# Performance work log

Measured on AMD Instinct MI355X. Metric: run time of the kernel, lower is better.

## Reference

```python
import jax, jax.numpy as jnp
import numpy as np

B, S, H, NH = 32, 512, 768, 12
EC, EU = 4, 4
CAP = 1.0
DH = H // NH
CAPACITY = int(CAP * B / EC)  # Switch-style capacity per common expert


def setup_inputs() -> dict:
    key = jax.random.key(0)
    ks = jax.random.split(key, 10)
    s = 0.02
    E = EC + EU  # experts stacked: [0:EC]=common, [EC:]=unique
    return {
        "hidden_states": jax.random.normal(ks[0], (B, S, H), jnp.float32),
        "attention_mask": jnp.zeros((B, S), jnp.float32),  # additive mask
        "Wq": jax.random.normal(ks[1], (E, H, H), jnp.float32) * s,
        "bq": jnp.zeros((E, H), jnp.float32),
        "Wk": jax.random.normal(ks[2], (E, H, H), jnp.float32) * s,
        "bk": jnp.zeros((E, H), jnp.float32),
        "Wv": jax.random.normal(ks[3], (E, H, H), jnp.float32) * s,
        "bv": jnp.zeros((E, H), jnp.float32),
        "Wo": jax.random.normal(ks[4], (E, H, H), jnp.float32) * s,
        "bo": jnp.zeros((E, H), jnp.float32),
        "Wsc": jax.random.normal(ks[5], (H, EC), jnp.float32) * s,
        "bsc": jnp.zeros((EC,), jnp.float32),
        "Wsu": jax.random.normal(ks[6], (H, EU), jnp.float32) * s,
        "bsu": jnp.zeros((EU,), jnp.float32),
    }


def reference(hidden_states, attention_mask, Wq, bq, Wk, bk, Wv, bv, Wo, bo,
              Wsc, bsc, Wsu, bsu):
    # ---- common routing (per-sequence top-1 over mean-pooled tokens) ----
    h_mean = hidden_states.mean(axis=1)                       # [B,H]
    pc = jax.nn.softmax(h_mean @ Wsc + bsc, axis=-1)          # [B,EC]
    rc = jnp.argmax(pc, axis=-1)                              # [B]
    pc_max = jnp.max(pc, axis=-1)                             # [B]
    # capacity drop: within each expert keep the CAPACITY highest-prob seqs
    order = jnp.argsort(-pc_max)                              # global desc sort
    oh = jax.nn.one_hot(rc[order], EC, dtype=jnp.int32)       # [B,EC]
    rank = jnp.take_along_axis(jnp.cumsum(oh, axis=0), rc[order][:, None], 1)[:, 0]
    kept = jnp.zeros((B,), bool).at[order].set(rank <= CAPACITY)

    # ---- unique routing for dropped sequences (mean is per-sequence, so
    #      computing on the full batch and masking matches torch) ----
    pu = jax.nn.softmax(h_mean @ Wsu + bsu, axis=-1)          # [B,EU]
    ru = jnp.argmax(pu, axis=-1)
    pu_max = jnp.max(pu, axis=-1)

    # per-sequence expert index into stacked [EC+EU] expert params
    eidx = jnp.where(kept, rc, EC + ru)                       # [B]
    # scaling factor p/stop_grad(p): ==1 in fwd, routes grads to the gate
    scale = jnp.where(kept,
                      pc_max / jax.lax.stop_gradient(pc_max),
                      pu_max / jax.lax.stop_gradient(pu_max))

    # ---- gather-dispatch: per-sequence expert weights ----
    Wq_b, Wk_b, Wv_b, Wo_b = Wq[eidx], Wk[eidx], Wv[eidx], Wo[eidx]  # [B,H,H]
    bq_b, bk_b, bv_b, bo_b = bq[eidx], bk[eidx], bv[eidx], bo[eidx]  # [B,H]

    def heads(t):  # [B,S,H] -> [B,NH,S,DH]
        return t.reshape(B, S, NH, DH).transpose(0, 2, 1, 3)

    q = heads(jnp.einsum('bsh,bhd->bsd', hidden_states, Wq_b) + bq_b[:, None, :])
    k = heads(jnp.einsum('bsh,bhd->bsd', hidden_states, Wk_b) + bk_b[:, None, :])
    v = heads(jnp.einsum('bsh,bhd->bsd', hidden_states, Wv_b) + bv_b[:, None, :])

    scores = jnp.einsum('bhsd,bhtd->bhst', q, k) / np.float32(np.sqrt(DH))
    scores = scores + attention_mask[:, None, None, :]        # additive mask
    attn = jax.nn.softmax(scores, axis=-1)
    ctx = jnp.einsum('bhst,bhtd->bhsd', attn, v)
    ctx = ctx.transpose(0, 2, 1, 3).reshape(B, S, H)

    out = jnp.einsum('bsh,bhd->bsd', ctx, Wo_b) + bo_b[:, None, :]
    return out * scale[:, None, None]
```

## Files before the change

kernel.cpp:

```cpp
#include <hip/hip_runtime.h>
#include <hip/hip_bf16.h>

#define B_ 32
#define S_ 512
#define H_ 768
#define NH_ 12
#define DH_ 64
#define EC_ 4
#define CAPN_ 8

using short8  = __attribute__((ext_vector_type(8))) short;
using floatx4 = __attribute__((ext_vector_type(4))) float;
using uint2v  = __attribute__((ext_vector_type(2))) unsigned;
using bf16 = __hip_bfloat16;

__device__ __forceinline__ void gl_lds16(const void* g, void* l) {
  __builtin_amdgcn_global_load_lds(
      (const __attribute__((address_space(1))) unsigned int*)g,
      (__attribute__((address_space(3))) unsigned int*)l, 16, 0, 0);
}

__device__ __forceinline__ unsigned pk2(float lo, float hi) {
  __hip_bfloat162 h = __float22bfloat162_rn(make_float2(lo, hi));
  unsigned r;
  __builtin_memcpy(&r, &h, 4);
  return r;
}

__global__ void k_mean_convert(const float* __restrict__ X, bf16* __restrict__ Xh,
                               float* __restrict__ partial) {
  int idx = blockIdx.x * 256 + threadIdx.x;
  int b = idx / H_, h = idx - b * H_;
  int s0 = blockIdx.y * 64;
  size_t base = ((size_t)b * S_ + s0) * H_ + h;
  float sum = 0.f;
#pragma unroll 8
  for (int s = 0; s < 64; ++s) {
    float v = X[base + (size_t)s * H_];
    Xh[base + (size_t)s * H_] = __float2bfloat16(v);
    sum += v;
  }
  partial[(size_t)blockIdx.y * (B_ * H_) + idx] = sum;
}

__global__ void k_mean_reduce(const float* __restrict__ partial, float* __restrict__ hmean) {
  int idx = blockIdx.x * 256 + threadIdx.x;
  float s = 0.f;
#pragma unroll
  for (int c = 0; c < 8; ++c) s += partial[(size_t)c * (B_ * H_) + idx];
  hmean[idx] = s * (1.f / 512.f);
}

__global__ void k_wt(const float* __restrict__ Wq, const float* __restrict__ Wk,
                     const float* __restrict__ Wv, const float* __restrict__ Wo,
                     bf16* __restrict__ Wt) {
  __shared__ float tile[32][33];
  int z = blockIdx.z;
  const float* Wbase = (z < 8 ? Wq : z < 16 ? Wk : z < 24 ? Wv : Wo) + (size_t)(z & 7) * H_ * H_;
  int k0 = blockIdx.x * 32, n0 = blockIdx.y * 32;
  int tj = threadIdx.x & 31, ti = threadIdx.x >> 5;
#pragma unroll
  for (int r = 0; r < 4; ++r)
    tile[ti + r * 8][tj] = Wbase[(size_t)(k0 + ti + r * 8) * H_ + n0 + tj];
  __syncthreads();
  bf16* out = Wt + (size_t)z * H_ * H_;
#pragma unroll
  for (int r = 0; r < 4; ++r)
    out[(size_t)(n0 + ti + r * 8) * H_ + k0 + tj] = __float2bfloat16(tile[tj][ti + r * 8]);
}

__global__ void k_gate(const float* __restrict__ hmean,
                       const float* __restrict__ Wsc, const float* __restrict__ bsc,
                       const float* __restrict__ Wsu, const float* __restrict__ bsu,
                       float* __restrict__ logits) {
  int b = blockIdx.x;
  int t = threadIdx.x;
  int g = t >> 3, p = t & 7;
  const float* hm = hmean + (size_t)b * H_;
  const float* w;
  float bias;
  if (g < 4) { w = Wsc + g; bias = bsc[g]; }
  else       { w = Wsu + (g - 4); bias = bsu[g - 4]; }
  float acc = 0.f;
  for (int j = p; j < H_; j += 8) acc += hm[j] * w[j * 4];
  acc += __shfl_xor(acc, 1);
  acc += __shfl_xor(acc, 2);
  acc += __shfl_xor(acc, 4);
  if (p == 0) logits[b * 8 + g] = acc + bias;
}

__global__ void k_route2(const float* __restrict__ logits, int* __restrict__ eidx) {
  __shared__ float pcmax[B_];
  __shared__ int rc_s[B_], ru_s[B_];
  int t = threadIdx.x;
  if (t < B_) {
    float lg[8];
#pragma unroll
    for (int e = 0; e < 8; ++e) lg[e] = logits[t * 8 + e];
    float m = lg[0]; int a = 0;
    for (int e = 1; e < 4; ++e) if (lg[e] > m) { m = lg[e]; a = e; }
    float s = 0.f;
    for (int e = 0; e < 4; ++e) s += expf(lg[e] - m);
    pcmax[t] = 1.f / s;
    rc_s[t] = a;
    float mu = lg[4]; int au = 0;
    for (int e = 1; e < 4; ++e) if (lg[4 + e] > mu) { mu = lg[4 + e]; au = e; }
    ru_s[t] = au;
  }
  __syncthreads();
  if (t == 0) {
    bool used[B_], kept[B_];
    int cnt[EC_] = {0, 0, 0, 0};
    for (int i = 0; i < B_; ++i) used[i] = false;
    for (int i = 0; i < B_; ++i) {
      int best = 0; float bv = -1e30f;
      for (int j = 0; j < B_; ++j)
        if (!used[j] && pcmax[j] > bv) { bv = pcmax[j]; best = j; }
      used[best] = true;
      kept[best] = (++cnt[rc_s[best]] <= CAPN_);
    }
    for (int i = 0; i < B_; ++i)
      eidx[i] = kept[i] ? rc_s[i] : EC_ + ru_s[i];
  }
}

template <int OMODE>
__global__ __launch_bounds__(256) void k_gemm(
    const bf16* __restrict__ A, const bf16* __restrict__ Wt,
    const float* __restrict__ bias0, const float* __restrict__ bias1,
    const float* __restrict__ bias2,
    void* out0, void* out1, void* out2,
    const int* __restrict__ eidx, int mat0) {
  __shared__ __align__(16) char lds[2][32768];
  int bz = blockIdx.z;
  int b = blockIdx.y;
  int e = eidx[b];
  int mtile = blockIdx.x & 3, ntile = blockIdx.x >> 2;
  int m0 = mtile * 128, n0 = ntile * 128;
  const bf16* Ab = A + (size_t)b * S_ * H_;
  const bf16* Wb = Wt + (size_t)((mat0 + bz) * 8 + e) * H_ * H_;
  const float* bias = ((bz == 0) ? bias0 : (bz == 1) ? bias1 : bias2) + (size_t)e * H_;
  void* outp = (bz == 0) ? out0 : (bz == 1) ? out1 : out2;

  int t = threadIdx.x, lane = t & 63, w = t >> 6;
  int wm = (w & 1) * 64, wn = (w >> 1) * 64;
  int lm = lane & 15, lq = lane >> 4;

  auto stage = [&](int kt) {
    char* buf = lds[kt & 1];
#pragma unroll
    for (int r = 0; r < 8; ++r) {
      int c = t + r * 256;
      const bf16* g;
      if (c < 1024) {
        int mm = c >> 3, pos = c & 7, kc = pos ^ (mm & 7);
        g = Ab + (size_t)(m0 + mm) * H_ + kt * 64 + kc * 8;
      } else {
        int c2 = c - 1024;
        int nn = c2 >> 3, pos = c2 & 7, kc = pos ^ (nn & 7);
        g = Wb + (size_t)(n0 + nn) * H_ + kt * 64 + kc * 8;
      }
      gl_lds16(g, buf + (size_t)c * 16);
    }
  };

  floatx4 acc[4][4] = {};
  stage(0);
  __syncthreads();
  for (int kt = 0; kt < 12; ++kt) {
    if (kt < 11) stage(kt + 1);
    const char* cur = lds[kt & 1];
#pragma unroll
    for (int kf = 0; kf < 2; ++kf) {
      int kc = kf * 4 + lq;
      short8 af[4], bf[4];
#pragma unroll
      for (int mf = 0; mf < 4; ++mf) {
        int mm = wm + mf * 16 + lm;
        af[mf] = *(const short8*)(cur + ((size_t)(mm * 8 + (kc ^ (mm & 7)))) * 16);
      }
#pragma unroll
      for (int nf = 0; nf < 4; ++nf) {
        int nn = wn + nf * 16 + lm;
        bf[nf] = *(const short8*)(cur + 16384 + ((size_t)(nn * 8 + (kc ^ (nn & 7)))) * 16);
      }
#pragma unroll
      for (int mf = 0; mf < 4; ++mf)
#pragma unroll
        for (int nf = 0; nf < 4; ++nf)
          acc[mf][nf] = __builtin_amdgcn_mfma_f32_16x16x32_bf16(af[mf], bf[nf], acc[mf][nf], 0, 0, 0);
    }
    if (kt < 11) __syncthreads();
  }
#pragma unroll
  for (int mf = 0; mf < 4; ++mf) {
#pragma unroll
    for (int nf = 0; nf < 4; ++nf) {
      int n = n0 + wn + nf * 16 + lm;
      float bv = bias[n];
      int mrow = m0 + wm + mf * 16 + lq * 4;
      size_t rowbase = ((size_t)b * S_ + mrow) * H_ + n;
#pragma unroll
      for (int r = 0; r < 4; ++r) {
        float v = acc[mf][nf][r] + bv;
        if (OMODE == 0) {
          if (bz == 2) {
            int s = mrow + r;
            ((bf16*)outp)[((size_t)(b * NH_ + (n >> 6))) * 32768 +
                          (size_t)(s >> 3) * 512 + (n & 63) * 8 + (s & 7)] =
                __float2bfloat16(v);
          } else {
            ((bf16*)outp)[rowbase + (size_t)r * H_] = __float2bfloat16(v);
          }
        } else {
          ((float*)outp)[rowbase + (size_t)r * H_] = v;
        }
      }
    }
  }
}

__global__ __launch_bounds__(256, 3) void k_attn(
    const bf16* __restrict__ Q, const bf16* __restrict__ K,
    const bf16* __restrict__ Vt, const float* __restrict__ mask,
    bf16* __restrict__ Ctx) {
  int bh = blockIdx.x;
  int b = bh / NH_, h = bh - b * NH_;
  int t = threadIdx.x, lane = t & 63, w = t >> 6;
  int lm = lane & 15, lq = lane >> 4;
  int q0 = blockIdx.y * 128 + w * 32;

  short8 qf[2][2];
#pragma unroll
  for (int mf = 0; mf < 2; ++mf)
#pragma unroll
    for (int kf = 0; kf < 2; ++kf)
      qf[mf][kf] = *(const short8*)(Q + ((size_t)(b * S_ + q0 + mf * 16 + lm)) * H_ +
                                    h * DH_ + kf * 32 + lq * 8);

  int kr = ((lm >> 2) << 3) + (lm & 3);
  const int koff[4] = {0, 4, 32, 36};
  const bf16* kbase = K + ((size_t)(b * S_) + kr) * H_ + h * DH_ + lq * 8;
  const bf16* vtb = Vt + ((size_t)(b * NH_ + h)) * 32768;
  const float* mbase = mask + (size_t)b * S_ + lq * 8;

  floatx4 oacc[2][4] = {};
  float m_[2] = {-1e30f, -1e30f}, l_[2] = {0.f, 0.f};

  for (int kt = 0; kt < 8; ++kt) {
    floatx4 sT[2][4] = {};
#pragma unroll
    for (int kf = 0; kf < 2; ++kf) {
      short8 kb4[4];
#pragma unroll
      for (int nf = 0; nf < 4; ++nf)
        kb4[nf] = *(const short8*)(kbase + (size_t)(kt * 64 + koff[nf]) * H_ + kf * 32);
#pragma unroll
      for (int mf = 0; mf < 2; ++mf)
#pragma unroll
        for (int nf = 0; nf < 4; ++nf)
          sT[mf][nf] = __builtin_amdgcn_mfma_f32_16x16x32_bf16(kb4[nf], qf[mf][kf], sT[mf][nf], 0, 0, 0);
    }
    short8 vf[2][4];
#pragma unroll
    for (int kf = 0; kf < 2; ++kf)
#pragma unroll
      for (int nf = 0; nf < 4; ++nf)
        vf[kf][nf] = *(const short8*)(vtb + (size_t)(kt * 8 + kf * 4 + lq) * 512 +
                                      (nf * 16 + lm) * 8);
    const floatx4* mp = (const floatx4*)(mbase + kt * 64);
    floatx4 mv[4] = {mp[0], mp[1], mp[8], mp[9]};

    short8 pf[2][2];
#pragma unroll
    for (int mf = 0; mf < 2; ++mf) {
      float p[4][4];
#pragma unroll
      for (int nf = 0; nf < 4; ++nf)
#pragma unroll
        for (int r = 0; r < 4; ++r)
          p[nf][r] = sT[mf][nf][r] * 0.125f + mv[nf][r];
      float t01 = fmaxf(fmaxf(fmaxf(p[0][0], p[0][1]), fmaxf(p[0][2], p[0][3])),
                        fmaxf(fmaxf(p[1][0], p[1][1]), fmaxf(p[1][2], p[1][3])));
      float t23 = fmaxf(fmaxf(fmaxf(p[2][0], p[2][1]), fmaxf(p[2][2], p[2][3])),
                        fmaxf(fmaxf(p[3][0], p[3][1]), fmaxf(p[3][2], p[3][3])));
      float tm = fmaxf(t01, t23);
      tm = fmaxf(tm, __shfl_xor(tm, 16));
      tm = fmaxf(tm, __shfl_xor(tm, 32));
      float mn = fmaxf(m_[mf], tm);
      float a = __expf(m_[mf] - mn);
      m_[mf] = mn;
      float ps = 0.f;
#pragma unroll
      for (int nf = 0; nf < 4; ++nf)
#pragma unroll
        for (int r = 0; r < 4; ++r) {
          p[nf][r] = __expf(p[nf][r] - mn);
          ps += p[nf][r];
        }
      ps += __shfl_xor(ps, 16);
      ps += __shfl_xor(ps, 32);
      l_[mf] = l_[mf] * a + ps;
#pragma unroll
      for (int nf = 0; nf < 4; ++nf) oacc[mf][nf] *= a;
      union { short8 s8; unsigned u[4]; } pku;
      pku.u[0] = pk2(p[0][0], p[0][1]); pku.u[1] = pk2(p[0][2], p[0][3]);
      pku.u[2] = pk2(p[1][0], p[1][1]); pku.u[3] = pk2(p[1][2], p[1][3]);
      pf[mf][0] = pku.s8;
      pku.u[0] = pk2(p[2][0], p[2][1]); pku.u[1] = pk2(p[2][2], p[2][3]);
      pku.u[2] = pk2(p[3][0], p[3][1]); pku.u[3] = pk2(p[3][2], p[3][3]);
      pf[mf][1] = pku.s8;
    }
#pragma unroll
    for (int kf = 0; kf < 2; ++kf)
#pragma unroll
      for (int mf = 0; mf < 2; ++mf)
#pragma unroll
        for (int nf = 0; nf < 4; ++nf)
          oacc[mf][nf] = __builtin_amdgcn_mfma_f32_16x16x32_bf16(vf[kf][nf], pf[mf][kf], oacc[mf][nf], 0, 0, 0);
  }
#pragma unroll
  for (int mf = 0; mf < 2; ++mf) {
    float inv = 1.f / l_[mf];
    bf16* op = Ctx + ((size_t)(b * S_ + q0 + mf * 16 + lm)) * H_ + h * DH_ + lq * 4;
#pragma unroll
    for (int nf = 0; nf < 4; ++nf) {
      uint2v o;
      o.x = pk2(oacc[mf][nf][0] * inv, oacc[mf][nf][1] * inv);
      o.y = pk2(oacc[mf][nf][2] * inv, oacc[mf][nf][3] * inv);
      *(uint2v*)(op + nf * 16) = o;
    }
  }
}

extern "C" void kernel_launch(void* const* d_in, const int* in_sizes, int n_in,
                              void* d_out, int out_size, void* d_ws, size_t ws_size,
                              hipStream_t stream) {
  const float* X    = (const float*)d_in[0];
  const float* mask = (const float*)d_in[1];
  const float* Wq   = (const float*)d_in[2];
  const float* bq   = (const float*)d_in[3];
  const float* Wk   = (const float*)d_in[4];
  const float* bk   = (const float*)d_in[5];
  const float* Wv   = (const float*)d_in[6];
  const float* bv   = (const float*)d_in[7];
  const float* Wo   = (const float*)d_in[8];
  const float* bo   = (const float*)d_in[9];
  const float* Wsc  = (const float*)d_in[10];
  const float* bsc  = (const float*)d_in[11];
  const float* Wsu  = (const float*)d_in[12];
  const float* bsu  = (const float*)d_in[13];

  char* ws = (char*)d_ws;
  int*   eidx    = (int*)ws;
  float* logits  = (float*)(ws + 128);
  float* partial = (float*)(ws + 1280);
  float* hmean   = (float*)(ws + 787712);
  bf16*  Xh      = (bf16*)(ws + 886016);
  bf16*  Wt      = (bf16*)(ws + 26051840);
  bf16*  qb      = (bf16*)(ws + 63800576);
  bf16*  kb      = (bf16*)(ws + 88966400);
  bf16*  Vt      = (bf16*)(ws + 114132224);
  bf16*  ctx     = Xh;

  k_mean_convert<<<dim3(96, 8), 256, 0, stream>>>(X, Xh, partial);
  k_mean_reduce<<<96, 256, 0, stream>>>(partial, hmean);
  k_wt<<<dim3(24, 24, 32), 256, 0, stream>>>(Wq, Wk, Wv, Wo, Wt);
  k_gate<<<B_, 64, 0, stream>>>(hmean, Wsc, bsc, Wsu, bsu, logits);
  k_route2<<<1, 64, 0, stream>>>(logits, eidx);
  k_gemm<0><<<dim3(24, 32, 3), 256, 0, stream>>>(Xh, Wt, bq, bk, bv,
                                                 (void*)qb, (void*)kb, (void*)Vt, eidx, 0);
  k_attn<<<dim3(B_ * NH_, 4), 256, 0, stream>>>(qb, kb, Vt, mask, ctx);
  k_gemm<1><<<dim3(24, 32, 1), 256, 0, stream>>>(ctx, Wt, bo, bo, bo,
                                                 d_out, d_out, d_out, eidx, 3);
}
```

Baseline: 475.0 us.

## Rewrite expert GEMM as 256x256 tiles with 8 waves and interleaved staging

The batched expert GEMM now uses 256x256 output tiles with 512-thread workgroups, a 128 KB double-buffered LDS, and a 1-D grid remapped so consecutive workgroups land on different XCDs. Global-to-LDS loads are split into four quarter stages interleaved with MFMA sub-blocks, using explicit vmcnt waits, barriers and setprio to overlap memory with compute. The aim is more data reuse per tile and fewer load stalls. In exchange, register pressure and LDS use per workgroup rise, and the grid is smaller, which can hurt occupancy and tail balance.

Result: no change. 467.2 us (-1.6%).

```diff
diff --git a/kernel.cpp b/kernel.cpp
--- a/kernel.cpp
+++ b/kernel.cpp
@@ -13,6 +13,8 @@
 using floatx4 = __attribute__((ext_vector_type(4))) float;
 using uint2v  = __attribute__((ext_vector_type(2))) unsigned;
 using bf16 = __hip_bfloat16;
+
+#define VMCNT(n) asm volatile("s_waitcnt vmcnt(" #n ")" ::: "memory")
 
 __device__ __forceinline__ void gl_lds16(const void* g, void* l) {
   __builtin_amdgcn_global_load_lds(
@@ -125,86 +127,137 @@
 }
 
 template <int OMODE>
-__global__ __launch_bounds__(256) void k_gemm(
+__global__ __launch_bounds__(512, 2) void k_gemm(
     const bf16* __restrict__ A, const bf16* __restrict__ Wt,
     const float* __restrict__ bias0, const float* __restrict__ bias1,
     const float* __restrict__ bias2,
     void* out0, void* out1, void* out2,
-    const int* __restrict__ eidx, int mat0) {
-  __shared__ __align__(16) char lds[2][32768];
-  int bz = blockIdx.z;
-  int b = blockIdx.y;
+    const int* __restrict__ eidx, int mat0, int nm) {
+  __shared__ __align__(16) char lds[2][65536];
+  int nwg = gridDim.x;
+  int wg = blockIdx.x;
+  int f = (wg & 7) * (nwg >> 3) + (wg >> 3);
+  int b = f / (6 * nm);
+  int r0 = f - b * 6 * nm;
+  int mat = r0 / 6;
+  int tile = r0 - mat * 6;
+  int m0 = (tile & 1) * 256, n0 = (tile >> 1) * 256;
   int e = eidx[b];
-  int mtile = blockIdx.x & 3, ntile = blockIdx.x >> 2;
-  int m0 = mtile * 128, n0 = ntile * 128;
   const bf16* Ab = A + (size_t)b * S_ * H_;
-  const bf16* Wb = Wt + (size_t)((mat0 + bz) * 8 + e) * H_ * H_;
-  const float* bias = ((bz == 0) ? bias0 : (bz == 1) ? bias1 : bias2) + (size_t)e * H_;
-  void* outp = (bz == 0) ? out0 : (bz == 1) ? out1 : out2;
+  const bf16* Wb = Wt + (size_t)((mat0 + mat) * 8 + e) * H_ * H_;
+  const float* bias = ((mat == 0) ? bias0 : (mat == 1) ? bias1 : bias2) + (size_t)e * H_;
+  void* outp = (mat == 0) ? out0 : (mat == 1) ? out1 : out2;
 
   int t = threadIdx.x, lane = t & 63, w = t >> 6;
-  int wm = (w & 1) * 64, wn = (w >> 1) * 64;
+  int wm = w >> 2, wn = w & 3;
   int lm = lane & 15, lq = lane >> 4;
 
-  auto stage = [&](int kt) {
+  auto stage_pair = [&](int p, int kt) {
     char* buf = lds[kt & 1];
 #pragma unroll
-    for (int r = 0; r < 8; ++r) {
-      int c = t + r * 256;
-      const bf16* g;
-      if (c < 1024) {
-        int mm = c >> 3, pos = c & 7, kc = pos ^ (mm & 7);
-        g = Ab + (size_t)(m0 + mm) * H_ + kt * 64 + kc * 8;
-      } else {
-        int c2 = c - 1024;
-        int nn = c2 >> 3, pos = c2 & 7, kc = pos ^ (nn & 7);
-        g = Wb + (size_t)(n0 + nn) * H_ + kt * 64 + kc * 8;
+    for (int s = 0; s < 2; ++s) {
+      int idx = t + s * 512;
+      int row, isB;
+      if (p == 0)      { row = (idx >> 9) * 128 +      ((idx & 511) >> 3); isB = 0; }
+      else if (p == 1) { row = (idx >> 9) * 128 + 64 + ((idx & 511) >> 3); isB = 0; }
+      else if (p == 2) { row = (idx >> 8) * 64 +       ((idx & 255) >> 3); isB = 1; }
+      else             { row = (idx >> 8) * 64 + 32 +  ((idx & 255) >> 3); isB = 1; }
+      int pos = idx & 7;
+      int kc = pos ^ (row & 7);
+      const bf16* g = (isB ? Wb + (size_t)(n0 + row) * H_
+                           : Ab + (size_t)(m0 + row) * H_) + kt * 64 + kc * 8;
+      gl_lds16(g, buf + isB * 32768 + row * 128 + pos * 16);
+    }
+  };
+
+  short8 af[4][2], bf0[2][2], bf1[2][2];
+  auto ldA = [&](const char* cur, int mh) {
+#pragma unroll
+    for (int mf = 0; mf < 4; ++mf) {
+      int mm = wm * 128 + mh * 64 + mf * 16 + lm;
+#pragma unroll
+      for (int kf = 0; kf < 2; ++kf) {
+        int kc = kf * 4 + lq;
+        af[mf][kf] = *(const short8*)(cur + ((size_t)(mm * 8 + (kc ^ (mm & 7)))) * 16);
       }
-      gl_lds16(g, buf + (size_t)c * 16);
     }
   };
-
-  floatx4 acc[4][4] = {};
-  stage(0);
-  __syncthreads();
-  for (int kt = 0; kt < 12; ++kt) {
-    if (kt < 11) stage(kt + 1);
-    const char* cur = lds[kt & 1];
-#pragma unroll
-    for (int kf = 0; kf < 2; ++kf) {
-      int kc = kf * 4 + lq;
-      short8 af[4], bf[4];
-#pragma unroll
-      for (int mf = 0; mf < 4; ++mf) {
-        int mm = wm + mf * 16 + lm;
-        af[mf] = *(const short8*)(cur + ((size_t)(mm * 8 + (kc ^ (mm & 7)))) * 16);
+  auto ldB = [&](const char* cur, int nh, short8 bfr[2][2]) {
+#pragma unroll
+    for (int nf = 0; nf < 2; ++nf) {
+      int nn = wn * 64 + nh * 32 + nf * 16 + lm;
+#pragma unroll
+      for (int kf = 0; kf < 2; ++kf) {
+        int kc = kf * 4 + lq;
+        bfr[nf][kf] = *(const short8*)(cur + 32768 + ((size_t)(nn * 8 + (kc ^ (nn & 7)))) * 16);
       }
-#pragma unroll
-      for (int nf = 0; nf < 4; ++nf) {
-        int nn = wn + nf * 16 + lm;
-        bf[nf] = *(const short8*)(cur + 16384 + ((size_t)(nn * 8 + (kc ^ (nn & 7)))) * 16);
-      }
+    }
+  };
+
+  floatx4 acc[8][4] = {};
+  auto mfma16 = [&](short8 bfr[2][2], int mh, int nh) {
+    __builtin_amdgcn_s_setprio(1);
+#pragma unroll
+    for (int kf = 0; kf < 2; ++kf)
 #pragma unroll
       for (int mf = 0; mf < 4; ++mf)
 #pragma unroll
-        for (int nf = 0; nf < 4; ++nf)
-          acc[mf][nf] = __builtin_amdgcn_mfma_f32_16x16x32_bf16(af[mf], bf[nf], acc[mf][nf], 0, 0, 0);
-    }
-    if (kt < 11) __syncthreads();
-  }
-#pragma unroll
-  for (int mf = 0; mf < 4; ++mf) {
-#pragma unroll
-    for (int nf = 0; nf < 4; ++nf) {
-      int n = n0 + wn + nf * 16 + lm;
-      float bv = bias[n];
-      int mrow = m0 + wm + mf * 16 + lq * 4;
+        for (int nf = 0; nf < 2; ++nf)
+          acc[mh * 4 + mf][nh * 2 + nf] = __builtin_amdgcn_mfma_f32_16x16x32_bf16(
+              af[mf][kf], bfr[nf][kf], acc[mh * 4 + mf][nh * 2 + nf], 0, 0, 0);
+    __builtin_amdgcn_s_setprio(0);
+  };
+
+  stage_pair(0, 0); stage_pair(2, 0); stage_pair(3, 0); stage_pair(1, 0);
+  VMCNT(0);
+  __builtin_amdgcn_s_barrier();
+  __builtin_amdgcn_sched_barrier(0);
+
+  for (int j = 0; j < 11; ++j) {
+    const char* cur = lds[j & 1];
+    stage_pair(0, j + 1);
+    VMCNT(6); __builtin_amdgcn_s_barrier(); __builtin_amdgcn_sched_barrier(0);
+    ldB(cur, 0, bf0); ldA(cur, 0);
+    mfma16(bf0, 0, 0);
+    stage_pair(2, j + 1);
+    VMCNT(6); __builtin_amdgcn_s_barrier(); __builtin_amdgcn_sched_barrier(0);
+    ldB(cur, 1, bf1);
+    mfma16(bf1, 0, 1);
+    stage_pair(3, j + 1);
+    VMCNT(6); __builtin_amdgcn_s_barrier(); __builtin_amdgcn_sched_barrier(0);
+    ldA(cur, 1);
+    mfma16(bf1, 1, 1);
+    stage_pair(1, j + 1);
+    mfma16(bf0, 1, 0);
+    __builtin_amdgcn_s_barrier(); __builtin_amdgcn_sched_barrier(0);
+  }
+  {
+    const char* cur = lds[1];
+    VMCNT(4); __builtin_amdgcn_s_barrier(); __builtin_amdgcn_sched_barrier(0);
+    ldB(cur, 0, bf0); ldA(cur, 0);
+    mfma16(bf0, 0, 0);
+    VMCNT(2); __builtin_amdgcn_s_barrier(); __builtin_amdgcn_sched_barrier(0);
+    ldB(cur, 1, bf1);
+    mfma16(bf1, 0, 1);
+    VMCNT(0); __builtin_amdgcn_s_barrier(); __builtin_amdgcn_sched_barrier(0);
+    ldA(cur, 1);
+    mfma16(bf1, 1, 1);
+    mfma16(bf0, 1, 0);
+  }
+
+#pragma unroll
+  for (int mi = 0; mi < 8; ++mi) {
+#pragma unroll
+    for (int ni = 0; ni < 4; ++ni) {
+      int n = n0 + wn * 64 + ni * 16 + lm;
+      float bvv = bias[n];
+      int mrow = m0 + wm * 128 + mi * 16 + lq * 4;
       size_t rowbase = ((size_t)b * S_ + mrow) * H_ + n;
 #pragma unroll
       for (int r = 0; r < 4; ++r) {
-        float v = acc[mf][nf][r] + bv;
+        float v = acc[mi][ni][r] + bvv;
         if (OMODE == 0) {
-          if (bz == 2) {
+          if (mat == 2) {
             int s = mrow + r;
             ((bf16*)outp)[((size_t)(b * NH_ + (n >> 6))) * 32768 +
                           (size_t)(s >> 3) * 512 + (n & 63) * 8 + (s & 7)] =
@@ -368,9 +421,9 @@
   k_wt<<<dim3(24, 24, 32), 256, 0, stream>>>(Wq, Wk, Wv, Wo, Wt);
   k_gate<<<B_, 64, 0, stream>>>(hmean, Wsc, bsc, Wsu, bsu, logits);
   k_route2<<<1, 64, 0, stream>>>(logits, eidx);
-  k_gemm<0><<<dim3(24, 32, 3), 256, 0, stream>>>(Xh, Wt, bq, bk, bv,
-                                                 (void*)qb, (void*)kb, (void*)Vt, eidx, 0);
+  k_gemm<0><<<dim3(576), 512, 0, stream>>>(Xh, Wt, bq, bk, bv,
+                                           (void*)qb, (void*)kb, (void*)Vt, eidx, 0, 3);
   k_attn<<<dim3(B_ * NH_, 4), 256, 0, stream>>>(qb, kb, Vt, mask, ctx);
-  k_gemm<1><<<dim3(24, 32, 1), 256, 0, stream>>>(ctx, Wt, bo, bo, bo,
-                                                 d_out, d_out, d_out, eidx, 3);
-}
+  k_gemm<1><<<dim3(192), 512, 0, stream>>>(ctx, Wt, bo, bo, bo,
+                                           d_out, d_out, d_out, eidx, 3, 1);
+}
```

## Triple-buffer GEMM K-loop with smaller K tiles, vmcnt waits, and XCD-aware block remap

Applied to the files above, without the earlier changes.

Reworks the expert GEMM mainloop to use K=32 tiles in a three-stage LDS ring with prefetch distance two. Raw s_waitcnt vmcnt plus s_barrier replace __syncthreads, so one stage of loads can stay in flight during compute. Shrinking LDS to 48KB with launch_bounds(256,3) is meant to allow three blocks per CU. The grid becomes 1-D with a remap that gives each XCD (blockIdx mod 8) a contiguous set of batches and matrices, aiming for better L2 reuse of the same expert weights and activations. The cost is twice as many barriers per tile and hand-written wait counts that must match the issued loads exactly.

Result: faster. 454.2 us (-4.4%).

```diff
diff --git a/kernel.cpp b/kernel.cpp
--- a/kernel.cpp
+++ b/kernel.cpp
@@ -13,6 +13,8 @@
 using floatx4 = __attribute__((ext_vector_type(4))) float;
 using uint2v  = __attribute__((ext_vector_type(2))) unsigned;
 using bf16 = __hip_bfloat16;
+
+#define VMCNT(n) asm volatile("s_waitcnt vmcnt(" #n ")" ::: "memory")
 
 __device__ __forceinline__ void gl_lds16(const void* g, void* l) {
   __builtin_amdgcn_global_load_lds(
@@ -124,74 +126,84 @@
   }
 }
 
-template <int OMODE>
-__global__ __launch_bounds__(256) void k_gemm(
+template <int OMODE, int NM>
+__global__ __launch_bounds__(256, 3) void k_gemm(
     const bf16* __restrict__ A, const bf16* __restrict__ Wt,
     const float* __restrict__ bias0, const float* __restrict__ bias1,
     const float* __restrict__ bias2,
     void* out0, void* out1, void* out2,
     const int* __restrict__ eidx, int mat0) {
-  __shared__ __align__(16) char lds[2][32768];
-  int bz = blockIdx.z;
-  int b = blockIdx.y;
+  __shared__ __align__(16) char lds[3][16384];
+  const int nwg = 96 * NM * 8;
+  int wg = blockIdx.x;
+  int f = (wg & 7) * (nwg >> 3) + (wg >> 3);
+  int b = f / (24 * NM);
+  int r0 = f - b * 24 * NM;
+  int mat = r0 / 24;
+  int tile = r0 - mat * 24;
+  int m0 = (tile & 3) * 128, n0 = (tile >> 2) * 128;
   int e = eidx[b];
-  int mtile = blockIdx.x & 3, ntile = blockIdx.x >> 2;
-  int m0 = mtile * 128, n0 = ntile * 128;
   const bf16* Ab = A + (size_t)b * S_ * H_;
-  const bf16* Wb = Wt + (size_t)((mat0 + bz) * 8 + e) * H_ * H_;
-  const float* bias = ((bz == 0) ? bias0 : (bz == 1) ? bias1 : bias2) + (size_t)e * H_;
-  void* outp = (bz == 0) ? out0 : (bz == 1) ? out1 : out2;
+  const bf16* Wb = Wt + (size_t)((mat0 + mat) * 8 + e) * H_ * H_;
+  const float* bias = ((mat == 0) ? bias0 : (mat == 1) ? bias1 : bias2) + (size_t)e * H_;
+  void* outp = (mat == 0) ? out0 : (mat == 1) ? out1 : out2;
 
   int t = threadIdx.x, lane = t & 63, w = t >> 6;
   int wm = (w & 1) * 64, wn = (w >> 1) * 64;
   int lm = lane & 15, lq = lane >> 4;
 
-  auto stage = [&](int kt) {
-    char* buf = lds[kt & 1];
-#pragma unroll
-    for (int r = 0; r < 8; ++r) {
+  auto stage = [&](char* buf, int kt) {
+#pragma unroll
+    for (int r = 0; r < 4; ++r) {
       int c = t + r * 256;
-      const bf16* g;
-      if (c < 1024) {
-        int mm = c >> 3, pos = c & 7, kc = pos ^ (mm & 7);
-        g = Ab + (size_t)(m0 + mm) * H_ + kt * 64 + kc * 8;
-      } else {
-        int c2 = c - 1024;
-        int nn = c2 >> 3, pos = c2 & 7, kc = pos ^ (nn & 7);
-        g = Wb + (size_t)(n0 + nn) * H_ + kt * 64 + kc * 8;
-      }
+      int isB = c >> 9;
+      int cc = c & 511;
+      int row = cc >> 2, pos = cc & 3;
+      int kc = pos ^ (row & 3);
+      const bf16* g = (isB ? Wb + (size_t)(n0 + row) * H_
+                           : Ab + (size_t)(m0 + row) * H_) + kt * 32 + kc * 8;
       gl_lds16(g, buf + (size_t)c * 16);
     }
   };
 
   floatx4 acc[4][4] = {};
-  stage(0);
-  __syncthreads();
-  for (int kt = 0; kt < 12; ++kt) {
-    if (kt < 11) stage(kt + 1);
-    const char* cur = lds[kt & 1];
-#pragma unroll
-    for (int kf = 0; kf < 2; ++kf) {
-      int kc = kf * 4 + lq;
-      short8 af[4], bf[4];
-#pragma unroll
-      for (int mf = 0; mf < 4; ++mf) {
-        int mm = wm + mf * 16 + lm;
-        af[mf] = *(const short8*)(cur + ((size_t)(mm * 8 + (kc ^ (mm & 7)))) * 16);
-      }
-#pragma unroll
-      for (int nf = 0; nf < 4; ++nf) {
-        int nn = wn + nf * 16 + lm;
-        bf[nf] = *(const short8*)(cur + 16384 + ((size_t)(nn * 8 + (kc ^ (nn & 7)))) * 16);
-      }
-#pragma unroll
-      for (int mf = 0; mf < 4; ++mf)
-#pragma unroll
-        for (int nf = 0; nf < 4; ++nf)
-          acc[mf][nf] = __builtin_amdgcn_mfma_f32_16x16x32_bf16(af[mf], bf[nf], acc[mf][nf], 0, 0, 0);
-    }
-    if (kt < 11) __syncthreads();
-  }
+  stage(lds[0], 0);
+  stage(lds[1], 1);
+  VMCNT(4);
+  __builtin_amdgcn_s_barrier();
+  __builtin_amdgcn_sched_barrier(0);
+
+  int cb = 0;
+  for (int kt = 0; kt < 24; ++kt) {
+    if (kt < 22) {
+      int pb = cb + 2; if (pb >= 3) pb -= 3;
+      stage(lds[pb], kt + 2);
+    }
+    const char* cur = lds[cb];
+    short8 af[4], bfr[4];
+#pragma unroll
+    for (int mf = 0; mf < 4; ++mf) {
+      int mm = wm + mf * 16 + lm;
+      af[mf] = *(const short8*)(cur + mm * 64 + ((lq ^ (mm & 3)) * 16));
+    }
+#pragma unroll
+    for (int nf = 0; nf < 4; ++nf) {
+      int nn = wn + nf * 16 + lm;
+      bfr[nf] = *(const short8*)(cur + 8192 + nn * 64 + ((lq ^ (nn & 3)) * 16));
+    }
+#pragma unroll
+    for (int mf = 0; mf < 4; ++mf)
+#pragma unroll
+      for (int nf = 0; nf < 4; ++nf)
+        acc[mf][nf] = __builtin_amdgcn_mfma_f32_16x16x32_bf16(af[mf], bfr[nf], acc[mf][nf], 0, 0, 0);
+    if (kt < 23) {
+      if (kt < 22) { VMCNT(4); } else { VMCNT(0); }
+      __builtin_amdgcn_s_barrier();
+      __builtin_amdgcn_sched_barrier(0);
+    }
+    ++cb; if (cb == 3) cb = 0;
+  }
+
 #pragma unroll
   for (int mf = 0; mf < 4; ++mf) {
 #pragma unroll
@@ -204,7 +216,7 @@
       for (int r = 0; r < 4; ++r) {
         float v = acc[mf][nf][r] + bv;
         if (OMODE == 0) {
-          if (bz == 2) {
+          if (mat == 2) {
             int s = mrow + r;
             ((bf16*)outp)[((size_t)(b * NH_ + (n >> 6))) * 32768 +
                           (size_t)(s >> 3) * 512 + (n & 63) * 8 + (s & 7)] =
@@ -368,9 +380,9 @@
   k_wt<<<dim3(24, 24, 32), 256, 0, stream>>>(Wq, Wk, Wv, Wo, Wt);
   k_gate<<<B_, 64, 0, stream>>>(hmean, Wsc, bsc, Wsu, bsu, logits);
   k_route2<<<1, 64, 0, stream>>>(logits, eidx);
-  k_gemm<0><<<dim3(24, 32, 3), 256, 0, stream>>>(Xh, Wt, bq, bk, bv,
-                                                 (void*)qb, (void*)kb, (void*)Vt, eidx, 0);
+  k_gemm<0, 3><<<dim3(2304), 256, 0, stream>>>(Xh, Wt, bq, bk, bv,
+                                               (void*)qb, (void*)kb, (void*)Vt, eidx, 0);
   k_attn<<<dim3(B_ * NH_, 4), 256, 0, stream>>>(qb, kb, Vt, mask, ctx);
-  k_gemm<1><<<dim3(24, 32, 1), 256, 0, stream>>>(ctx, Wt, bo, bo, bo,
-                                                 d_out, d_out, d_out, eidx, 3);
-}
+  k_gemm<1, 1><<<dim3(768), 256, 0, stream>>>(ctx, Wt, bo, bo, bo,
+                                              d_out, d_out, d_out, eidx, 3);
+}
```
